# Performance work log

Hardware: AMD Instinct MI355X
Metric: run time of the kernel (lower is better)

Reference implementation:

```python
import jax, jax.numpy as jnp
import numpy as np

B, C, H, W = 16, 128, 48, 48
C4 = C // 4
N = H * W
BN_EPS = 1e-5


def conv_bn_relu(x, w, gamma, beta, mean, var):
    # 1x1 conv (no bias) as channel contraction, then eval-mode BatchNorm, then ReLU
    y = jnp.einsum('bchw,oc->bohw', x, w)
    scale = gamma / jnp.sqrt(var + BN_EPS)
    y = y * scale[None, :, None, None] + (beta - mean * scale)[None, :, None, None]
    return jax.nn.relu(y)


def setup_inputs() -> dict:
    key = jax.random.key(0)
    ks = jax.random.split(key, 16)
    inp = {
        'x_en': jax.random.normal(ks[0], (B, C, H, W), dtype=jnp.float32),
        'x_de': jax.random.normal(ks[1], (B, C, H, W), dtype=jnp.float32),
        'x_cat': jax.random.normal(ks[2], (B, 2 * C, H, W), dtype=jnp.float32),
        # Get_KQ: Conv2d(C -> C/4, 1x1, no bias) + BN(C/4) (shared for K and Q)
        'w_kq': jax.random.normal(ks[3], (C4, C), dtype=jnp.float32) * 0.05,
        'kq_gamma': jax.random.normal(ks[4], (C4,), dtype=jnp.float32) * 0.1 + 1.0,
        'kq_beta': jax.random.normal(ks[5], (C4,), dtype=jnp.float32) * 0.1,
        'kq_mean': jax.random.normal(ks[6], (C4,), dtype=jnp.float32) * 0.1,
        'kq_var': jax.random.uniform(ks[7], (C4,), dtype=jnp.float32) + 0.5,
        # Get_V: Conv2d(C -> C, 1x1, no bias) + BN(C)
        'w_v': jax.random.normal(ks[8], (C, C), dtype=jnp.float32) * 0.05,
        'v_gamma': jax.random.normal(ks[9], (C,), dtype=jnp.float32) * 0.1 + 1.0,
        'v_beta': jax.random.normal(ks[10], (C,), dtype=jnp.float32) * 0.1,
        'v_mean': jax.random.normal(ks[11], (C,), dtype=jnp.float32) * 0.1,
        'v_var': jax.random.uniform(ks[12], (C,), dtype=jnp.float32) + 0.5,
        # reduce_channels: Conv2d(2C -> C, 1x1, no bias) + BN(C)
        'w_red': jax.random.normal(ks[13], (C, 2 * C), dtype=jnp.float32) * 0.05,
        'red_gamma': jax.random.normal(ks[14], (C,), dtype=jnp.float32) * 0.1 + 1.0,
        'red_beta': jax.random.normal(ks[15], (C,), dtype=jnp.float32) * 0.1,
        'red_mean': jax.random.normal(jax.random.fold_in(key, 100), (C,), dtype=jnp.float32) * 0.1,
        'red_var': jax.random.uniform(jax.random.fold_in(key, 101), (C,), dtype=jnp.float32) + 0.5,
    }
    return inp


def reference(x_en, x_de, x_cat,
              w_kq, kq_gamma, kq_beta, kq_mean, kq_var,
              w_v, v_gamma, v_beta, v_mean, v_var,
              w_red, red_gamma, red_beta, red_mean, red_var):
    Kf = conv_bn_relu(x_en, w_kq, kq_gamma, kq_beta, kq_mean, kq_var).reshape(B, C4, N)
    Qf = conv_bn_relu(x_de, w_kq, kq_gamma, kq_beta, kq_mean, kq_var).reshape(B, C4, N)
    # KQ[b, n, m] = sum_k K[b, k, n] * Q[b, k, m]  -> [B, N, N]
    KQ = jnp.einsum('bkn,bkm->bnm', Kf, Qf)
    # GLOBAL softmax over the flattened N*N map (per batch), not per row
    A = jax.nn.softmax(KQ.reshape(B, N * N), axis=1).reshape(B, N, N)
    x = conv_bn_relu(x_cat, w_red, red_gamma, red_beta, red_mean, red_var)
    V = conv_bn_relu(x, w_v, v_gamma, v_beta, v_mean, v_var).reshape(B, C, N)
    # FeatureMap[b, c, n] = sum_m V[b, c, m] * A[b, n, m]
    feat = jnp.einsum('bcm,bnm->bcn', V, A).reshape(B, C, H, W)
    return jnp.concatenate([x, feat], axis=1)
```

## Files before the change

### kernel.cpp

```cpp
#include <hip/hip_runtime.h>
#include <math.h>

#define C    128
#define C4   32
#define NN   2304
#define BN_EPS 1e-5f
#define NEG_INF -3.402823466e38f
#define LOG2E 1.4426950408889634f

typedef short bf16x8 __attribute__((ext_vector_type(8)));
typedef float f32x4 __attribute__((ext_vector_type(4)));

#define SOFT_BARRIER() asm volatile("s_waitcnt lgkmcnt(0)\n\ts_barrier" ::: "memory")

__device__ inline unsigned short f2bf(float f) {
    unsigned int u = __float_as_uint(f);
    u += 0x7fffu + ((u >> 16) & 1u);
    return (unsigned short)(u >> 16);
}

__device__ inline unsigned int pk2bf(float a, float b) {
#if __has_builtin(__builtin_amdgcn_cvt_pk_bf16_f32)
    typedef __bf16 bf2 __attribute__((ext_vector_type(2)));
    bf2 v = __builtin_amdgcn_cvt_pk_bf16_f32(a, b);
    return __builtin_bit_cast(unsigned int, v);
#else
    unsigned int ua = __float_as_uint(a); ua += 0x7fffu + ((ua >> 16) & 1u);
    unsigned int ub = __float_as_uint(b); ub += 0x7fffu + ((ub >> 16) & 1u);
    return __builtin_amdgcn_perm(ub, ua, 0x07060302u);
#endif
}

__device__ inline float fexp2(float x) {
#if __has_builtin(__builtin_amdgcn_exp2f)
    return __builtin_amdgcn_exp2f(x);
#else
    return __expf(x * 0.69314718055994531f);
#endif
}


__global__ __launch_bounds__(256) void k_wprep(
    const float* __restrict__ wkq, const float* __restrict__ kq_g,
    const float* __restrict__ kq_b, const float* __restrict__ kq_m,
    const float* __restrict__ kq_v,
    const float* __restrict__ wv, const float* __restrict__ v_g,
    const float* __restrict__ v_b, const float* __restrict__ v_m,
    const float* __restrict__ v_v,
    const float* __restrict__ wred, const float* __restrict__ red_g,
    const float* __restrict__ red_b, const float* __restrict__ red_m,
    const float* __restrict__ red_v,
    unsigned short* __restrict__ wkq_bf, unsigned short* __restrict__ wv_bf,
    unsigned short* __restrict__ wred_bf,
    float* __restrict__ kq_sh, float* __restrict__ v_sh, float* __restrict__ red_sh)
{
    const int t = blockIdx.x * 256 + threadIdx.x;
    if (t < 4096) {
        const int o = t >> 7;
        const float sc = kq_g[o] * rsqrtf(kq_v[o] + BN_EPS);
        wkq_bf[t] = f2bf(wkq[t] * sc);
        if ((t & 127) == 0) kq_sh[o] = kq_b[o] - kq_m[o] * sc;
    } else if (t < 4096 + 16384) {
        const int e = t - 4096;
        const int o = e >> 7;
        const float sc = v_g[o] * rsqrtf(v_v[o] + BN_EPS);
        wv_bf[e] = f2bf(wv[e] * sc);
        if ((e & 127) == 0) v_sh[o] = v_b[o] - v_m[o] * sc;
    } else if (t < 4096 + 16384 + 32768) {
        const int e = t - 20480;
        const int o = e >> 8;
        const float sc = red_g[o] * rsqrtf(red_v[o] + BN_EPS);
        wred_bf[e] = f2bf(wred[e] * sc);
        if ((e & 255) == 0) red_sh[o] = red_b[o] - red_m[o] * sc;
    }
}

__global__ __launch_bounds__(256) void k_kq(
    const float* __restrict__ x0, const float* __restrict__ x1,
    const unsigned short* __restrict__ wbf, const float* __restrict__ shift,
    unsigned short* __restrict__ Kt, unsigned short* __restrict__ Qt)
{
    constexpr int NTILE = 128, R = 8;
    __shared__ unsigned short Xs[2][NTILE][40];

    const int tid = threadIdx.x;
    const int w = tid >> 6, lane = tid & 63;
    const int quad = lane >> 4, l16 = lane & 15;
    const int b = blockIdx.y, n0 = blockIdx.x * NTILE;
    const int nbase = w * 32;

    const float* xin = (blockIdx.z ? x1 : x0) + (size_t)b * C * NN;
    const int p = tid & 15, g = tid >> 4;

    f32x4 acc[2][2];
#pragma unroll
    for (int mt = 0; mt < 2; mt++)
#pragma unroll
        for (int nt = 0; nt < 2; nt++) acc[mt][nt] = (f32x4){0.f, 0.f, 0.f, 0.f};

    const float* xrb = xin + n0 + g * R;
    float av[R], bv[R];
    {
        const float* xr = xrb + (size_t)(2 * p) * NN;
#pragma unroll
        for (int i4 = 0; i4 < R; i4 += 4) {
            *(float4*)&av[i4] = *(const float4*)&xr[i4];
            *(float4*)&bv[i4] = *(const float4*)&xr[NN + i4];
        }
    }

    for (int k = 0; k < 4; ++k) {
        unsigned int uu[R];
#pragma unroll
        for (int i = 0; i < R; i++) uu[i] = pk2bf(av[i], bv[i]);
        if (k < 3) {
            const float* xr = xrb + (size_t)((k + 1) * 32 + 2 * p) * NN;
#pragma unroll
            for (int i4 = 0; i4 < R; i4 += 4) {
                *(float4*)&av[i4] = *(const float4*)&xr[i4];
                *(float4*)&bv[i4] = *(const float4*)&xr[NN + i4];
            }
        }
        unsigned int* Xw = (unsigned int*)Xs[k & 1];
#pragma unroll
        for (int i = 0; i < R; i++)
            Xw[(g * R + i) * 20 + p] = uu[i];
        SOFT_BARRIER();
        bf16x8 af[2];
#pragma unroll
        for (int mt = 0; mt < 2; mt++)
            af[mt] = *(const bf16x8*)&wbf[(size_t)(mt * 16 + l16) * C + k * 32 + quad * 8];
#pragma unroll
        for (int nt = 0; nt < 2; nt++) {
            const bf16x8 bfr = *(const bf16x8*)&Xs[k & 1][nbase + nt * 16 + l16][quad * 8];
#pragma unroll
            for (int mt = 0; mt < 2; mt++)
                acc[mt][nt] = __builtin_amdgcn_mfma_f32_16x16x32_bf16(af[mt], bfr, acc[mt][nt], 0, 0, 0);
        }
    }

    unsigned short* ob16 = blockIdx.z ? Qt : Kt;
    const float osc = blockIdx.z ? 1.f : LOG2E;
#pragma unroll
    for (int mt = 0; mt < 2; mt++)
#pragma unroll
        for (int nt = 0; nt < 2; nt++)
#pragma unroll
            for (int r = 0; r < 4; r++) {
                const int o = mt * 16 + quad * 4 + r;
                const int n = n0 + nbase + nt * 16 + l16;
                const float sh = shift[o];
                ob16[((size_t)b * NN + n) * 32 + o] =
                    f2bf(fmaxf(acc[mt][nt][r] + sh, 0.f) * osc);
            }
}

__global__ __launch_bounds__(256) void k_redv(
    const float* __restrict__ xcat,
    const unsigned short* __restrict__ wred_bf, const float* __restrict__ red_sh,
    const unsigned short* __restrict__ wv_bf,  const float* __restrict__ v_sh,
    float* __restrict__ out, unsigned short* __restrict__ Vf)
{
    __shared__ unsigned short Xs[2][48][40];
    __shared__ unsigned int   Xv[64 * 49];

    const int tid = threadIdx.x;
    const int w = tid >> 6, lane = tid & 63;
    const int quad = lane >> 4, l16 = lane & 15;
    const int b = blockIdx.y, n0 = blockIdx.x * 48;
    const float* xin = xcat + (size_t)b * 2 * C * NN;
    const int p = tid & 15, g = tid >> 4;

    f32x4 acc[2][3];
#pragma unroll
    for (int mt = 0; mt < 2; mt++)
#pragma unroll
        for (int nt = 0; nt < 3; nt++) acc[mt][nt] = (f32x4){0.f, 0.f, 0.f, 0.f};

    float4 av, bv;
    if (g < 12) {
        const float* xr = xin + (size_t)(2 * p) * NN + n0 + g * 4;
        av = *(const float4*)&xr[0];
        bv = *(const float4*)&xr[NN];
    }

    for (int k = 0; k < 8; ++k) {
        if (g < 12) {
            const unsigned int u0 = pk2bf(av.x, bv.x);
            const unsigned int u1 = pk2bf(av.y, bv.y);
            const unsigned int u2 = pk2bf(av.z, bv.z);
            const unsigned int u3 = pk2bf(av.w, bv.w);
            if (k < 7) {
                const float* xr = xin + (size_t)((k + 1) * 32 + 2 * p) * NN + n0 + g * 4;
                av = *(const float4*)&xr[0];
                bv = *(const float4*)&xr[NN];
            }
            unsigned int* Xw = (unsigned int*)Xs[k & 1];
            Xw[(g * 4 + 0) * 20 + p] = u0;
            Xw[(g * 4 + 1) * 20 + p] = u1;
            Xw[(g * 4 + 2) * 20 + p] = u2;
            Xw[(g * 4 + 3) * 20 + p] = u3;
        }
        SOFT_BARRIER();
        bf16x8 af[2];
#pragma unroll
        for (int mt = 0; mt < 2; mt++)
            af[mt] = *(const bf16x8*)&wred_bf[(size_t)(w * 32 + mt * 16 + l16) * (2 * C) + k * 32 + quad * 8];
#pragma unroll
        for (int nt = 0; nt < 3; nt++) {
            const bf16x8 bfr = *(const bf16x8*)&Xs[k & 1][nt * 16 + l16][quad * 8];
#pragma unroll
            for (int mt = 0; mt < 2; mt++)
                acc[mt][nt] = __builtin_amdgcn_mfma_f32_16x16x32_bf16(af[mt], bfr, acc[mt][nt], 0, 0, 0);
        }
    }

    {
        float* ob = out + (size_t)b * (2 * C * NN);
#pragma unroll
        for (int mt = 0; mt < 2; mt++) {
            float sh[4];
#pragma unroll
            for (int r = 0; r < 4; r++) sh[r] = red_sh[w * 32 + mt * 16 + quad * 4 + r];
#pragma unroll
            for (int nt = 0; nt < 3; nt++) {
                const int n = n0 + nt * 16 + l16;
                float v[4];
#pragma unroll
                for (int r = 0; r < 4; r++) {
                    const int o = w * 32 + mt * 16 + quad * 4 + r;
                    v[r] = fmaxf(acc[mt][nt][r] + sh[r], 0.f);
                    ob[(size_t)o * NN + n] = v[r];
                }
                const int op0 = 16 * w + mt * 8 + quad * 2;
                Xv[(op0 + 0) * 49 + nt * 16 + l16] = pk2bf(v[0], v[1]);
                Xv[(op0 + 1) * 49 + nt * 16 + l16] = pk2bf(v[2], v[3]);
            }
        }
    }
    SOFT_BARRIER();

    f32x4 vacc[2][3];
#pragma unroll
    for (int mt = 0; mt < 2; mt++)
#pragma unroll
        for (int nt = 0; nt < 3; nt++) vacc[mt][nt] = (f32x4){0.f, 0.f, 0.f, 0.f};

    for (int c0 = 0; c0 < C; c0 += 32) {
        bf16x8 af[2];
#pragma unroll
        for (int mt = 0; mt < 2; mt++)
            af[mt] = *(const bf16x8*)&wv_bf[(size_t)(w * 32 + mt * 16 + l16) * C + c0 + quad * 8];
#pragma unroll
        for (int nt = 0; nt < 3; nt++) {
            const int col = nt * 16 + l16;
            const int cp0 = c0 / 2 + quad * 4;
            uint4 u;
            u.x = Xv[(cp0 + 0) * 49 + col];
            u.y = Xv[(cp0 + 1) * 49 + col];
            u.z = Xv[(cp0 + 2) * 49 + col];
            u.w = Xv[(cp0 + 3) * 49 + col];
            const bf16x8 bfr = __builtin_bit_cast(bf16x8, u);
#pragma unroll
            for (int mt = 0; mt < 2; mt++)
                vacc[mt][nt] = __builtin_amdgcn_mfma_f32_16x16x32_bf16(af[mt], bfr, vacc[mt][nt], 0, 0, 0);
        }
    }

#pragma unroll
    for (int mt = 0; mt < 2; mt++) {
        float sh[4];
#pragma unroll
        for (int r = 0; r < 4; r++) sh[r] = v_sh[w * 32 + mt * 16 + quad * 4 + r];
#pragma unroll
        for (int nt = 0; nt < 3; nt++)
#pragma unroll
            for (int r = 0; r < 4; r++) {
                const int o = w * 32 + mt * 16 + quad * 4 + r;
                const int n = n0 + nt * 16 + l16;
                Vf[((size_t)b * C + o) * NN + n] = f2bf(fmaxf(vacc[mt][nt][r] + sh[r], 0.f));
            }
    }
}

__global__ __launch_bounds__(256) void k_stats(
    const unsigned short* __restrict__ Kt, const unsigned short* __restrict__ Qt,
    float* __restrict__ bmax, float* __restrict__ bsum)
{
    const int tid = threadIdx.x;
    const int w = tid >> 6, lane = tid & 63;
    const int quad = lane >> 4, l16 = lane & 15;
    const int wg = blockIdx.x;
    const int xcd = wg & 7;
    const int slot = wg >> 3;
    const int b = xcd * 2 + slot / 324;
    const int tile = slot % 324;
    const int my = tile / 18, mx = tile % 18;
    const int n0 = mx * 128, m0 = my * 128;
    const unsigned short* Kb = Kt + (size_t)b * NN * 32;
    const unsigned short* Qb = Qt + (size_t)b * NN * 32;

    bf16x8 kf[8], qf[2];
#pragma unroll
    for (int nt = 0; nt < 8; nt++)
        kf[nt] = *(const bf16x8*)&Kb[(size_t)(n0 + nt * 16 + l16) * 32 + quad * 8];
#pragma unroll
    for (int mt = 0; mt < 2; mt++)
        qf[mt] = *(const bf16x8*)&Qb[(size_t)(m0 + w * 32 + mt * 16 + l16) * 32 + quad * 8];

    f32x4 s[16];
#pragma unroll
    for (int mt = 0; mt < 2; mt++)
#pragma unroll
        for (int nt = 0; nt < 8; nt++) {
            f32x4 z = (f32x4){0.f, 0.f, 0.f, 0.f};
            s[mt * 8 + nt] = __builtin_amdgcn_mfma_f32_16x16x32_bf16(qf[mt], kf[nt], z, 0, 0, 0);
        }

    float lmax = NEG_INF;
#pragma unroll
    for (int i = 0; i < 16; i++)
        lmax = fmaxf(lmax, fmaxf(fmaxf(s[i][0], s[i][1]), fmaxf(s[i][2], s[i][3])));
    float lsum = 0.f;
#pragma unroll
    for (int i = 0; i < 16; i++)
        lsum += fexp2(s[i][0] - lmax) + fexp2(s[i][1] - lmax) +
                fexp2(s[i][2] - lmax) + fexp2(s[i][3] - lmax);

#pragma unroll
    for (int off = 32; off > 0; off >>= 1) {
        const float omax = __shfl_xor(lmax, off);
        const float osum = __shfl_xor(lsum, off);
        const float nmax = fmaxf(lmax, omax);
        lsum = lsum * fexp2(lmax - nmax) + osum * fexp2(omax - nmax);
        lmax = nmax;
    }
    __shared__ float smax[4], ssum[4];
    if (lane == 0) { smax[w] = lmax; ssum[w] = lsum; }
    __syncthreads();
    if (tid == 0) {
        float M = smax[0], S = ssum[0];
        for (int i = 1; i < 4; i++) {
            const float nmax = fmaxf(M, smax[i]);
            S = S * fexp2(M - nmax) + ssum[i] * fexp2(smax[i] - nmax);
            M = nmax;
        }
        const int idx = (b * 18 + my) * 18 + mx;
        bmax[idx] = M;
        bsum[idx] = S;
    }
}

__global__ __launch_bounds__(256) void k_fin(
    const float* __restrict__ bmax, const float* __restrict__ bsum,
    float* __restrict__ Ms, float* __restrict__ Sinv)
{
    __shared__ float rmax[256], rsum[256];
    const int b = blockIdx.x, tid = threadIdx.x;
    float lmax = NEG_INF, lsum = 0.f;
    for (int i = tid; i < 324; i += 256) {
        const float m = bmax[b * 324 + i], s = bsum[b * 324 + i];
        const float nmax = fmaxf(lmax, m);
        lsum = lsum * fexp2(lmax - nmax) + s * fexp2(m - nmax);
        lmax = nmax;
    }
    rmax[tid] = lmax; rsum[tid] = lsum;
    __syncthreads();
    for (int st = 128; st > 0; st >>= 1) {
        if (tid < st) {
            const float m2 = rmax[tid + st], s2 = rsum[tid + st];
            const float nmax = fmaxf(rmax[tid], m2);
            rsum[tid] = rsum[tid] * fexp2(rmax[tid] - nmax) + s2 * fexp2(m2 - nmax);
            rmax[tid] = nmax;
        }
        __syncthreads();
    }
    if (tid == 0) { Ms[b] = rmax[0]; Sinv[b] = 1.f / rsum[0]; }
}

__global__ __launch_bounds__(256) void k_feat(
    const unsigned short* __restrict__ Kt, const unsigned short* __restrict__ Qt,
    const unsigned short* __restrict__ Vf, const float* __restrict__ Ms,
    const float* __restrict__ Sinv, float* __restrict__ out)
{
    __shared__ __align__(16) unsigned short Et[2][48][72];
    const int tid = threadIdx.x;
    const int w = tid >> 6, lane = tid & 63;
    const int quad = lane >> 4, l16 = lane & 15;
    const int wg = blockIdx.x;
    const int xcd = wg & 7;
    const int slot = wg >> 3;
    const int b = xcd * 2 + slot / 48;
    const int n0 = (slot % 48) * 48;
    const unsigned short* Kb = Kt + (size_t)b * NN * 32;
    const unsigned short* Qb = Qt + (size_t)b * NN * 32;
    const unsigned short* Vb = Vf + (size_t)b * C * NN;
    const float M = Ms[b], Si = Sinv[b];

    bf16x8 kf[3];
#pragma unroll
    for (int nt = 0; nt < 3; nt++)
        kf[nt] = *(const bf16x8*)&Kb[(size_t)(n0 + nt * 16 + l16) * 32 + quad * 8];

    f32x4 acc[2][3];
#pragma unroll
    for (int i = 0; i < 2; i++)
#pragma unroll
        for (int j = 0; j < 3; j++) acc[i][j] = (f32x4){0.f, 0.f, 0.f, 0.f};

    bf16x8 q0 = *(const bf16x8*)&Qb[(size_t)(w * 16 + l16) * 32 + quad * 8];
    bf16x8 vc[2][2];
#pragma unroll
    for (int ct = 0; ct < 2; ct++)
#pragma unroll
        for (int ks = 0; ks < 2; ks++)
            vc[ct][ks] = *(const bf16x8*)&Vb[(size_t)(w * 32 + ct * 16 + l16) * NN + ks * 32 + quad * 8];
    bf16x8 qc = *(const bf16x8*)&Qb[(size_t)(64 + w * 16 + l16) * 32 + quad * 8];
    {
        f32x4 s0[3];
#pragma unroll
        for (int nt = 0; nt < 3; nt++) {
            f32x4 z = (f32x4){0.f, 0.f, 0.f, 0.f};
            s0[nt] = __builtin_amdgcn_mfma_f32_16x16x32_bf16(q0, kf[nt], z, 0, 0, 0);
        }
#pragma unroll
        for (int nt = 0; nt < 3; nt++) {
            const unsigned int u0 = pk2bf(fexp2(s0[nt][0] - M), fexp2(s0[nt][1] - M));
            const unsigned int u1 = pk2bf(fexp2(s0[nt][2] - M), fexp2(s0[nt][3] - M));
            *(uint2*)&Et[0][nt * 16 + l16][w * 16 + quad * 4] = make_uint2(u0, u1);
        }
    }
    SOFT_BARRIER();

    for (int k = 0; k < 36; ++k) {
        const int cur = k & 1;
        const int mq = (k + 2 < 36 ? k + 2 : 0) * 64;
        const int mv = (k + 1 < 36 ? k + 1 : 0) * 64;
        bf16x8 qn = *(const bf16x8*)&Qb[(size_t)(mq + w * 16 + l16) * 32 + quad * 8];
        bf16x8 vn[2][2];
#pragma unroll
        for (int ct = 0; ct < 2; ct++)
#pragma unroll
            for (int ks = 0; ks < 2; ks++)
                vn[ct][ks] = *(const bf16x8*)&Vb[(size_t)(w * 32 + ct * 16 + l16) * NN + mv + ks * 32 + quad * 8];

        if (k < 35) {
            f32x4 s[3];
#pragma unroll
            for (int nt = 0; nt < 3; nt++) {
                f32x4 z = (f32x4){0.f, 0.f, 0.f, 0.f};
                s[nt] = __builtin_amdgcn_mfma_f32_16x16x32_bf16(qc, kf[nt], z, 0, 0, 0);
            }
#pragma unroll
            for (int nt = 0; nt < 3; nt++) {
                const unsigned int u0 = pk2bf(fexp2(s[nt][0] - M), fexp2(s[nt][1] - M));
                const unsigned int u1 = pk2bf(fexp2(s[nt][2] - M), fexp2(s[nt][3] - M));
                *(uint2*)&Et[cur ^ 1][nt * 16 + l16][w * 16 + quad * 4] = make_uint2(u0, u1);
            }
        }

#pragma unroll
        for (int ks = 0; ks < 2; ks++) {
#pragma unroll
            for (int nt = 0; nt < 3; nt++) {
                const bf16x8 ef = *(const bf16x8*)&Et[cur][nt * 16 + l16][ks * 32 + quad * 8];
                acc[0][nt] = __builtin_amdgcn_mfma_f32_16x16x32_bf16(vc[0][ks], ef, acc[0][nt], 0, 0, 0);
                acc[1][nt] = __builtin_amdgcn_mfma_f32_16x16x32_bf16(vc[1][ks], ef, acc[1][nt], 0, 0, 0);
            }
        }
        SOFT_BARRIER();
        qc = qn;
#pragma unroll
        for (int ct = 0; ct < 2; ct++)
#pragma unroll
            for (int ks = 0; ks < 2; ks++) vc[ct][ks] = vn[ct][ks];
    }

    float* ob = out + (size_t)b * 2 * C * NN + (size_t)C * NN + n0;
#pragma unroll
    for (int ct = 0; ct < 2; ct++)
#pragma unroll
        for (int nt = 0; nt < 3; nt++)
#pragma unroll
            for (int r = 0; r < 4; r++) {
                const int c = w * 32 + ct * 16 + quad * 4 + r;
                ob[(size_t)c * NN + nt * 16 + l16] = acc[ct][nt][r] * Si;
            }
}

extern "C" void kernel_launch(void* const* d_in, const int* in_sizes, int n_in,
                              void* d_out, int out_size, void* d_ws, size_t ws_size,
                              hipStream_t stream)
{
    const float* x_en   = (const float*)d_in[0];
    const float* x_de   = (const float*)d_in[1];
    const float* x_cat  = (const float*)d_in[2];
    const float* w_kq   = (const float*)d_in[3];
    const float* kq_g   = (const float*)d_in[4];
    const float* kq_b   = (const float*)d_in[5];
    const float* kq_m   = (const float*)d_in[6];
    const float* kq_v   = (const float*)d_in[7];
    const float* w_v    = (const float*)d_in[8];
    const float* v_g    = (const float*)d_in[9];
    const float* v_b    = (const float*)d_in[10];
    const float* v_m    = (const float*)d_in[11];
    const float* v_v    = (const float*)d_in[12];
    const float* w_red  = (const float*)d_in[13];
    const float* red_g  = (const float*)d_in[14];
    const float* red_b  = (const float*)d_in[15];
    const float* red_m  = (const float*)d_in[16];
    const float* red_v  = (const float*)d_in[17];

    unsigned short* Kt      = (unsigned short*)d_ws;
    unsigned short* Qt      = Kt + 1179648;
    unsigned short* Vf      = Qt + 1179648;
    unsigned short* wkq_bf  = Vf + 4718592;
    unsigned short* wv_bf   = wkq_bf + 4096;
    unsigned short* wred_bf = wv_bf + 16384;
    float* bmax = (float*)(wred_bf + 32768);
    float* bsum = bmax + 16 * 324;
    float* Ms   = bsum + 16 * 324;
    float* Sinv = Ms + 16;
    float* kq_sh  = Sinv + 16;
    float* v_sh   = kq_sh + 32;
    float* red_sh = v_sh + 128;
    float* out  = (float*)d_out;

    k_wprep<<<208, 256, 0, stream>>>(
        w_kq, kq_g, kq_b, kq_m, kq_v,
        w_v, v_g, v_b, v_m, v_v,
        w_red, red_g, red_b, red_m, red_v,
        wkq_bf, wv_bf, wred_bf, kq_sh, v_sh, red_sh);

    k_kq  <<<dim3(18, 16, 2), 256, 0, stream>>>(x_en, x_de, wkq_bf, kq_sh, Kt, Qt);
    k_redv<<<dim3(48, 16), 256, 0, stream>>>(x_cat, wred_bf, red_sh, wv_bf, v_sh, out, Vf);

    k_stats<<<5184, 256, 0, stream>>>(Kt, Qt, bmax, bsum);
    k_fin  <<<16, 256, 0, stream>>>(bmax, bsum, Ms, Sinv);
    k_feat <<<768, 256, 0, stream>>>(Kt, Qt, Vf, Ms, Sinv, out);
}
```

Baseline: 246.5 us.

## Double the m-tile per iteration in k_feat, halve barriers, add setprio around MFMAs

The fused exp/PV loop in k_feat now handles 128 key positions per iteration instead of 64, so each wave computes two 16-row Q tiles of scores and the shared E tile widens to 136 columns. This halves the number of loop iterations and block barriers. The V operands are no longer prefetched one iteration ahead; they are loaded at the top of the same iteration. The PV MFMA section is wrapped in s_setprio so waves issuing matrix ops get scheduling priority. The trade-offs are more LDS and registers per block and V load latency that is now exposed within each iteration.

```diff
diff --git a/kernel.cpp b/kernel.cpp
--- a/kernel.cpp
+++ b/kernel.cpp
@@ -383,7 +383,7 @@
     const unsigned short* __restrict__ Vf, const float* __restrict__ Ms,
     const float* __restrict__ Sinv, float* __restrict__ out)
 {
-    __shared__ __align__(16) unsigned short Et[2][48][72];
+    __shared__ __align__(16) unsigned short Et[2][48][136];
     const int tid = threadIdx.x;
     const int w = tid >> 6, lane = tid & 63;
     const int quad = lane >> 4, l16 = lane & 15;
@@ -408,59 +408,65 @@
 #pragma unroll
         for (int j = 0; j < 3; j++) acc[i][j] = (f32x4){0.f, 0.f, 0.f, 0.f};
 
-    bf16x8 q0 = *(const bf16x8*)&Qb[(size_t)(w * 16 + l16) * 32 + quad * 8];
-    bf16x8 vc[2][2];
-#pragma unroll
-    for (int ct = 0; ct < 2; ct++)
-#pragma unroll
-        for (int ks = 0; ks < 2; ks++)
-            vc[ct][ks] = *(const bf16x8*)&Vb[(size_t)(w * 32 + ct * 16 + l16) * NN + ks * 32 + quad * 8];
-    bf16x8 qc = *(const bf16x8*)&Qb[(size_t)(64 + w * 16 + l16) * 32 + quad * 8];
     {
-        f32x4 s0[3];
+        const bf16x8 q00 = *(const bf16x8*)&Qb[(size_t)(w * 32 + l16) * 32 + quad * 8];
+        const bf16x8 q01 = *(const bf16x8*)&Qb[(size_t)(w * 32 + 16 + l16) * 32 + quad * 8];
+        f32x4 s0[3], s1[3];
 #pragma unroll
         for (int nt = 0; nt < 3; nt++) {
             f32x4 z = (f32x4){0.f, 0.f, 0.f, 0.f};
-            s0[nt] = __builtin_amdgcn_mfma_f32_16x16x32_bf16(q0, kf[nt], z, 0, 0, 0);
+            s0[nt] = __builtin_amdgcn_mfma_f32_16x16x32_bf16(q00, kf[nt], z, 0, 0, 0);
+            s1[nt] = __builtin_amdgcn_mfma_f32_16x16x32_bf16(q01, kf[nt], z, 0, 0, 0);
         }
 #pragma unroll
         for (int nt = 0; nt < 3; nt++) {
-            const unsigned int u0 = pk2bf(fexp2(s0[nt][0] - M), fexp2(s0[nt][1] - M));
-            const unsigned int u1 = pk2bf(fexp2(s0[nt][2] - M), fexp2(s0[nt][3] - M));
-            *(uint2*)&Et[0][nt * 16 + l16][w * 16 + quad * 4] = make_uint2(u0, u1);
-        }
-    }
+            const unsigned int a0 = pk2bf(fexp2(s0[nt][0] - M), fexp2(s0[nt][1] - M));
+            const unsigned int a1 = pk2bf(fexp2(s0[nt][2] - M), fexp2(s0[nt][3] - M));
+            *(uint2*)&Et[0][nt * 16 + l16][w * 32 + quad * 4] = make_uint2(a0, a1);
+            const unsigned int b0 = pk2bf(fexp2(s1[nt][0] - M), fexp2(s1[nt][1] - M));
+            const unsigned int b1 = pk2bf(fexp2(s1[nt][2] - M), fexp2(s1[nt][3] - M));
+            *(uint2*)&Et[0][nt * 16 + l16][w * 32 + 16 + quad * 4] = make_uint2(b0, b1);
+        }
+    }
+    bf16x8 qc0 = *(const bf16x8*)&Qb[(size_t)(128 + w * 32 + l16) * 32 + quad * 8];
+    bf16x8 qc1 = *(const bf16x8*)&Qb[(size_t)(128 + w * 32 + 16 + l16) * 32 + quad * 8];
     SOFT_BARRIER();
 
-    for (int k = 0; k < 36; ++k) {
+    for (int k = 0; k < 18; ++k) {
         const int cur = k & 1;
-        const int mq = (k + 2 < 36 ? k + 2 : 0) * 64;
-        const int mv = (k + 1 < 36 ? k + 1 : 0) * 64;
-        bf16x8 qn = *(const bf16x8*)&Qb[(size_t)(mq + w * 16 + l16) * 32 + quad * 8];
-        bf16x8 vn[2][2];
+        const int m0 = k * 128;
+        const int mq = (k + 2 < 18 ? k + 2 : 0) * 128;
+        bf16x8 qn0 = *(const bf16x8*)&Qb[(size_t)(mq + w * 32 + l16) * 32 + quad * 8];
+        bf16x8 qn1 = *(const bf16x8*)&Qb[(size_t)(mq + w * 32 + 16 + l16) * 32 + quad * 8];
+        bf16x8 vc[2][4];
 #pragma unroll
         for (int ct = 0; ct < 2; ct++)
 #pragma unroll
-            for (int ks = 0; ks < 2; ks++)
-                vn[ct][ks] = *(const bf16x8*)&Vb[(size_t)(w * 32 + ct * 16 + l16) * NN + mv + ks * 32 + quad * 8];
-
-        if (k < 35) {
-            f32x4 s[3];
+            for (int ks = 0; ks < 4; ks++)
+                vc[ct][ks] = *(const bf16x8*)&Vb[(size_t)(w * 32 + ct * 16 + l16) * NN + m0 + ks * 32 + quad * 8];
+
+        if (k < 17) {
+            f32x4 s0[3], s1[3];
 #pragma unroll
             for (int nt = 0; nt < 3; nt++) {
                 f32x4 z = (f32x4){0.f, 0.f, 0.f, 0.f};
-                s[nt] = __builtin_amdgcn_mfma_f32_16x16x32_bf16(qc, kf[nt], z, 0, 0, 0);
+                s0[nt] = __builtin_amdgcn_mfma_f32_16x16x32_bf16(qc0, kf[nt], z, 0, 0, 0);
+                s1[nt] = __builtin_amdgcn_mfma_f32_16x16x32_bf16(qc1, kf[nt], z, 0, 0, 0);
             }
 #pragma unroll
             for (int nt = 0; nt < 3; nt++) {
-                const unsigned int u0 = pk2bf(fexp2(s[nt][0] - M), fexp2(s[nt][1] - M));
-                const unsigned int u1 = pk2bf(fexp2(s[nt][2] - M), fexp2(s[nt][3] - M));
-                *(uint2*)&Et[cur ^ 1][nt * 16 + l16][w * 16 + quad * 4] = make_uint2(u0, u1);
-            }
-        }
-
-#pragma unroll
-        for (int ks = 0; ks < 2; ks++) {
+                const unsigned int a0 = pk2bf(fexp2(s0[nt][0] - M), fexp2(s0[nt][1] - M));
+                const unsigned int a1 = pk2bf(fexp2(s0[nt][2] - M), fexp2(s0[nt][3] - M));
+                *(uint2*)&Et[cur ^ 1][nt * 16 + l16][w * 32 + quad * 4] = make_uint2(a0, a1);
+                const unsigned int b0 = pk2bf(fexp2(s1[nt][0] - M), fexp2(s1[nt][1] - M));
+                const unsigned int b1 = pk2bf(fexp2(s1[nt][2] - M), fexp2(s1[nt][3] - M));
+                *(uint2*)&Et[cur ^ 1][nt * 16 + l16][w * 32 + 16 + quad * 4] = make_uint2(b0, b1);
+            }
+        }
+
+        __builtin_amdgcn_s_setprio(1);
+#pragma unroll
+        for (int ks = 0; ks < 4; ks++) {
 #pragma unroll
             for (int nt = 0; nt < 3; nt++) {
                 const bf16x8 ef = *(const bf16x8*)&Et[cur][nt * 16 + l16][ks * 32 + quad * 8];
@@ -468,12 +474,10 @@
                 acc[1][nt] = __builtin_amdgcn_mfma_f32_16x16x32_bf16(vc[1][ks], ef, acc[1][nt], 0, 0, 0);
             }
         }
+        __builtin_amdgcn_s_setprio(0);
         SOFT_BARRIER();
-        qc = qn;
-#pragma unroll
-        for (int ct = 0; ct < 2; ct++)
-#pragma unroll
-            for (int ks = 0; ks < 2; ks++) vc[ct][ks] = vn[ct][ks];
+        qc0 = qn0;
+        qc1 = qn1;
     }
 
     float* ob = out + (size_t)b * 2 * C * NN + (size_t)C * NN + n0;
```

Result: no change. 249.2 us (+1.1%).
